# Kernel tuning notes

Hardware: AMD Instinct MI355X
Metric: run time of the kernel (lower is better)

The kernel has to match this reference:

```python
import jax, jax.numpy as jnp
import numpy as np

A, S, D, V = 128, 512, 768, 30522
NL, LW = 10, 5  # n label categories, words per category
MASK_ID = 103
NEG = -1e30


def setup_inputs() -> dict:
    key = jax.random.key(0)
    ks = jax.random.split(key, 12)
    scale = 0.02
    input_ids = jax.random.randint(ks[0], (A, S), 0, 30000)
    input_ids = jnp.where(input_ids == MASK_ID, MASK_ID + 1, input_ids)  # strip accidental masks
    mask_pos = jax.random.randint(ks[1], (A,), 1, 3)  # one [MASK] per row, before position 3
    input_ids = input_ids.at[jnp.arange(A), mask_pos].set(MASK_ID)
    length = jax.random.randint(ks[2], (A,), 1, 400)
    bert_out = jax.random.normal(ks[3], (A, S, D), jnp.float32)
    label_words = jax.random.randint(ks[4], (NL, LW), 0, V)
    return {
        "bert_out": bert_out,
        "input_ids": input_ids,
        "length": length,
        "label_words": label_words,
        "W_senti": jax.random.normal(ks[5], (2, D), jnp.float32) * scale,
        "b_senti": jnp.zeros((2,), jnp.float32),
        "W_dense": jax.random.normal(ks[6], (D, 2 * D), jnp.float32) * scale,
        "b_dense": jnp.zeros((D,), jnp.float32),
        "W_prob": jax.random.normal(ks[7], (V, D), jnp.float32) * scale,
        "b_prob": jnp.zeros((V,), jnp.float32),
        "W_lab": jax.random.normal(ks[8], (NL, 2, LW), jnp.float32) * scale,
    }


def reference(bert_out, input_ids, length, label_words,
              W_senti, b_senti, W_dense, b_dense, W_prob, b_prob, W_lab):
    a, s, d = bert_out.shape
    # pooler = [CLS] hidden state -> senti head (dropout is identity in eval)
    senti_out = bert_out[:, 0] @ W_senti.T + b_senti  # [A,2]

    # gather the (single) [MASK] token hidden state per sample
    mask_pos = jnp.argmax(input_ids == MASK_ID, axis=1)        # [A]
    mask_logit = bert_out[jnp.arange(a), mask_pos]             # [A,D]

    # ragged attention pool over bert_out[i, 3:3+length[i]] vectorized via masking
    pos = jnp.arange(s)
    valid = (pos[None, :] >= 3) & (pos[None, :] < 3 + length[:, None])  # [A,S]
    scores = jnp.einsum('asd,ad->as', bert_out, mask_logit)
    scores = jnp.where(valid, scores, NEG)
    w = jax.nn.softmax(scores, axis=1)                         # [A,S]
    att = jnp.einsum('as,asd->ad', w, bert_out)                # [A,D]

    x = jnp.concatenate([att, mask_logit], axis=-1)            # [A,2D]
    h = jnp.tanh(x @ W_dense.T + b_dense)                      # [A,D]
    p = jnp.tanh(h @ W_prob.T + b_prob)                        # [A,V]

    # per-category label-word gather + small no-bias linear, stacked on dim 2
    lp = p[:, label_words]                                     # [A,NL,LW]
    out = jnp.einsum('alw,lkw->akl', lp, W_lab)                # [A,2,NL]
    return senti_out, out
```

## Files before the change

### kernel.cpp

```cpp
#include <hip/hip_runtime.h>
#include <stdint.h>

#define A_ 128
#define S_ 512
#define D_ 768
#define MASKID 103

typedef short bf16x8_t __attribute__((ext_vector_type(8)));
typedef float floatx4_t __attribute__((ext_vector_type(4)));

__device__ __forceinline__ unsigned short f2bf(float f) {
    union { unsigned int u; float f; } v; v.f = f;
    unsigned int u = v.u;
    return (unsigned short)((u + 0x7fffu + ((u >> 16) & 1u)) >> 16);
}

__global__ __launch_bounds__(512) void attn_fused(
    const float* __restrict__ bert,
    const int* __restrict__ ids,
    const int* __restrict__ length,
    const int* __restrict__ label_words,
    const float* __restrict__ W_prob,
    const float* __restrict__ b_prob,
    const float* __restrict__ W_senti,
    const float* __restrict__ b_senti,
    unsigned short* __restrict__ ws_Wpw,
    float* __restrict__ ws_bp,
    unsigned short* __restrict__ ws_x,
    float* __restrict__ d_out)
{
    int bx = blockIdx.x;
    int tid = threadIdx.x;
    if (bx >= A_) {
        int r = bx - A_;
        if (r < 50) {
            int word = label_words[r];
            const float* src = W_prob + (size_t)word * D_;
            for (int j = tid; j < D_; j += 512) ws_Wpw[r * D_ + j] = f2bf(src[j]);
            if (tid == 0) ws_bp[r] = b_prob[word];
        } else {
            for (int j = tid; j < D_; j += 512) ws_Wpw[r * D_ + j] = 0;
            if (tid == 0) ws_bp[r] = 0.f;
        }
        return;
    }
    int a = bx;
    int wave = tid >> 6, lane = tid & 63;
    int d0 = lane * 12;

    __shared__ int s_minpos;
    __shared__ float red_m[8], red_l[8];
    __shared__ float red_acc[8][D_];
    __shared__ float s0[8], s1[8];

    if (tid == 0) s_minpos = S_;
    __syncthreads();
    if (ids[a * S_ + tid] == MASKID) atomicMin(&s_minpos, tid);
    __syncthreads();
    int mp = (s_minpos >= S_) ? 0 : s_minpos;

    const float* base = bert + (size_t)a * S_ * D_;

    float ml[12];
    {
        const float4* p = (const float4*)(base + (size_t)mp * D_ + d0);
        float4 v0 = p[0], v1 = p[1], v2 = p[2];
        ml[0]=v0.x; ml[1]=v0.y; ml[2]=v0.z; ml[3]=v0.w;
        ml[4]=v1.x; ml[5]=v1.y; ml[6]=v1.z; ml[7]=v1.w;
        ml[8]=v2.x; ml[9]=v2.y; ml[10]=v2.z; ml[11]=v2.w;
    }
    int len = length[a]; if (len > S_ - 3) len = S_ - 3;

    float m = -3.0e38f, l = 0.f;
    float acc[12];
#pragma unroll
    for (int k = 0; k < 12; k++) acc[k] = 0.f;

    for (int v = wave; v < len; v += 8) {
        int s = 3 + v;
        const float4* p = (const float4*)(base + (size_t)s * D_ + d0);
        float4 v0 = p[0], v1 = p[1], v2 = p[2];
        float r[12];
        r[0]=v0.x; r[1]=v0.y; r[2]=v0.z; r[3]=v0.w;
        r[4]=v1.x; r[5]=v1.y; r[6]=v1.z; r[7]=v1.w;
        r[8]=v2.x; r[9]=v2.y; r[10]=v2.z; r[11]=v2.w;
        float part = 0.f;
#pragma unroll
        for (int k = 0; k < 12; k++) part = fmaf(r[k], ml[k], part);
#pragma unroll
        for (int off = 32; off >= 1; off >>= 1)
            part += __shfl_xor(part, off, 64);
        float mn = fmaxf(m, part);
        float alpha = __expf(m - mn);
        float wgt = __expf(part - mn);
        l = l * alpha + wgt;
#pragma unroll
        for (int k = 0; k < 12; k++) acc[k] = fmaf(acc[k], alpha, wgt * r[k]);
        m = mn;
    }
    if (lane == 0) { red_m[wave] = m; red_l[wave] = l; }
#pragma unroll
    for (int k = 0; k < 12; k++) red_acc[wave][d0 + k] = acc[k];

    float p0 = 0.f, p1 = 0.f;
    for (int d = tid; d < D_; d += 512) {
        float b = base[d];
        p0 = fmaf(b, W_senti[d], p0);
        p1 = fmaf(b, W_senti[D_ + d], p1);
    }
#pragma unroll
    for (int off = 32; off >= 1; off >>= 1) {
        p0 += __shfl_xor(p0, off, 64);
        p1 += __shfl_xor(p1, off, 64);
    }
    if (lane == 0) { s0[wave] = p0; s1[wave] = p1; }
    __syncthreads();

    float M = red_m[0];
#pragma unroll
    for (int c = 1; c < 8; c++) M = fmaxf(M, red_m[c]);
    float fac[8]; float denom = 0.f;
#pragma unroll
    for (int c = 0; c < 8; c++) { fac[c] = __expf(red_m[c] - M); denom += fac[c] * red_l[c]; }
    float inv = 1.0f / fmaxf(denom, 1e-30f);

    const float* mrow = base + (size_t)mp * D_;
    for (int d = tid; d < D_; d += 512) {
        float s = 0.f;
#pragma unroll
        for (int c = 0; c < 8; c++) s += fac[c] * red_acc[c][d];
        ws_x[a * 1536 + d] = f2bf(s * inv);
        ws_x[a * 1536 + D_ + d] = f2bf(mrow[d]);
    }
    if (tid == 0) {
        float t0 = b_senti[0], t1 = b_senti[1];
#pragma unroll
        for (int c = 0; c < 8; c++) { t0 += s0[c]; t1 += s1[c]; }
        d_out[a * 2 + 0] = t0;
        d_out[a * 2 + 1] = t1;
    }
}

__global__ __launch_bounds__(256) void dense_kernel(
    const unsigned short* __restrict__ ws_x,
    const float* __restrict__ W_dense,
    const float* __restrict__ b_dense,
    unsigned short* __restrict__ ws_h)
{
    int tid = threadIdx.x;
    int wave = tid >> 6, lane = tid & 63;
    int r = lane & 15, q = lane >> 4;
    int tile_local = wave >> 1, kh = wave & 1;
    int T = blockIdx.x * 2 + tile_local;
    int m_t = T / 48, n_t = T % 48;
    const bf16x8_t* Ap = (const bf16x8_t*)(ws_x + (size_t)(m_t * 16 + r) * 1536 + kh * 768 + q * 8);
    const float* Bp = W_dense + (size_t)(n_t * 16 + r) * 1536 + kh * 768 + q * 8;
    floatx4_t acc = {0.f, 0.f, 0.f, 0.f};
#pragma unroll
    for (int kk = 0; kk < 24; kk++) {
        bf16x8_t av = Ap[kk * 4];
        float4 b0 = *(const float4*)(Bp + kk * 32);
        float4 b1 = *(const float4*)(Bp + kk * 32 + 4);
        bf16x8_t bv;
        bv[0] = (short)f2bf(b0.x); bv[1] = (short)f2bf(b0.y);
        bv[2] = (short)f2bf(b0.z); bv[3] = (short)f2bf(b0.w);
        bv[4] = (short)f2bf(b1.x); bv[5] = (short)f2bf(b1.y);
        bv[6] = (short)f2bf(b1.z); bv[7] = (short)f2bf(b1.w);
        acc = __builtin_amdgcn_mfma_f32_16x16x32_bf16(av, bv, acc, 0, 0, 0);
    }
    __shared__ float part[4][256];
#pragma unroll
    for (int reg = 0; reg < 4; reg++)
        part[wave][(q * 4 + reg) * 16 + r] = acc[reg];
    __syncthreads();
    for (int t = tid; t < 512; t += 256) {
        int tl = t >> 8, id2 = t & 255;
        float sum = part[tl * 2][id2] + part[tl * 2 + 1][id2];
        int T2 = blockIdx.x * 2 + tl;
        int mt2 = T2 / 48, nt2 = T2 % 48;
        int row = id2 >> 4, col = id2 & 15;
        int n = nt2 * 16 + col;
        float h = tanhf(sum + b_dense[n]);
        ws_h[(size_t)(mt2 * 16 + row) * 768 + n] = f2bf(h);
    }
}

__global__ __launch_bounds__(256) void label_kernel(
    const unsigned short* __restrict__ ws_h,
    const unsigned short* __restrict__ ws_Wpw,
    const float* __restrict__ ws_bp,
    const float* __restrict__ W_lab,
    float* __restrict__ d_out)
{
    int tid = threadIdx.x;
    int wave = tid >> 6, lane = tid & 63;
    int r = lane & 15, q = lane >> 4;
    int m_t = blockIdx.x;
    int n_t = wave;
    const bf16x8_t* Ap = (const bf16x8_t*)(ws_h + (size_t)(m_t * 16 + r) * 768 + q * 8);
    const bf16x8_t* Bp = (const bf16x8_t*)(ws_Wpw + (size_t)(n_t * 16 + r) * 768 + q * 8);
    floatx4_t acc = {0.f, 0.f, 0.f, 0.f};
#pragma unroll
    for (int kk = 0; kk < 24; kk++)
        acc = __builtin_amdgcn_mfma_f32_16x16x32_bf16(Ap[kk * 4], Bp[kk * 4], acc, 0, 0, 0);
    __shared__ float lp_s[16][64];
    int col = n_t * 16 + r;
    float bp = ws_bp[col];
#pragma unroll
    for (int reg = 0; reg < 4; reg++)
        lp_s[q * 4 + reg][col] = tanhf(acc[reg] + bp);
    __syncthreads();
    for (int t = tid; t < 320; t += 256) {
        int al = t / 20, rem = t % 20;
        int k = rem / 10, lb = rem % 10;
        float s = 0.f;
#pragma unroll
        for (int w = 0; w < 5; w++)
            s = fmaf(lp_s[al][lb * 5 + w], W_lab[(lb * 2 + k) * 5 + w], s);
        d_out[256 + (m_t * 16 + al) * 20 + rem] = s;
    }
}

extern "C" void kernel_launch(void* const* d_in, const int* in_sizes, int n_in,
                              void* d_out, int out_size, void* d_ws, size_t ws_size,
                              hipStream_t stream) {
    const float* bert    = (const float*)d_in[0];
    const int* ids       = (const int*)d_in[1];
    const int* length    = (const int*)d_in[2];
    const int* label_words = (const int*)d_in[3];
    const float* W_senti = (const float*)d_in[4];
    const float* b_senti = (const float*)d_in[5];
    const float* W_dense = (const float*)d_in[6];
    const float* b_dense = (const float*)d_in[7];
    const float* W_prob  = (const float*)d_in[8];
    const float* b_prob  = (const float*)d_in[9];
    const float* W_lab   = (const float*)d_in[10];
    float* out = (float*)d_out;

    char* ws = (char*)d_ws;
    unsigned short* ws_x   = (unsigned short*)(ws + 0);
    unsigned short* ws_h   = (unsigned short*)(ws + 393216);
    unsigned short* ws_Wpw = (unsigned short*)(ws + 589824);
    float*          ws_bp  = (float*)(ws + 688128);

    attn_fused<<<A_ + 64, 512, 0, stream>>>(bert, ids, length, label_words,
        W_prob, b_prob, W_senti, b_senti, ws_Wpw, ws_bp, ws_x, out);
    dense_kernel<<<192, 256, 0, stream>>>(ws_x, W_dense, b_dense, ws_h);
    label_kernel<<<8, 256, 0, stream>>>(ws_h, ws_Wpw, ws_bp, W_lab, out);
}
```

Measured before the change: 337.2 us.

## Split attention pooling across eight blocks per sample with a merge kernel

Splits each sample's ragged attention pool across 8 blocks of 256 threads (split-K flash-decoding style) instead of one 512-thread block per sample. Each block writes partial max, sum and accumulator to workspace, and a new merge kernel combines them and also computes the senti head. The aim is to fill the GPU's compute units while streaming bert_out, which 128 blocks cannot do. The cost is an extra kernel launch and a workspace round-trip for the partials, plus redundant mask-position scans in every split block.

```diff
diff --git a/kernel.cpp b/kernel.cpp
--- a/kernel.cpp
+++ b/kernel.cpp
@@ -15,47 +15,47 @@
     return (unsigned short)((u + 0x7fffu + ((u >> 16) & 1u)) >> 16);
 }
 
-__global__ __launch_bounds__(512) void attn_fused(
+__global__ __launch_bounds__(256) void attn_part(
     const float* __restrict__ bert,
     const int* __restrict__ ids,
     const int* __restrict__ length,
     const int* __restrict__ label_words,
     const float* __restrict__ W_prob,
     const float* __restrict__ b_prob,
-    const float* __restrict__ W_senti,
-    const float* __restrict__ b_senti,
     unsigned short* __restrict__ ws_Wpw,
     float* __restrict__ ws_bp,
-    unsigned short* __restrict__ ws_x,
-    float* __restrict__ d_out)
+    int* __restrict__ ws_mask_pos,
+    float* __restrict__ part_m,
+    float* __restrict__ part_l,
+    float* __restrict__ part_acc)
 {
     int bx = blockIdx.x;
     int tid = threadIdx.x;
-    if (bx >= A_) {
-        int r = bx - A_;
+    if (bx >= A_ * 8) {
+        int r = bx - A_ * 8;
         if (r < 50) {
             int word = label_words[r];
             const float* src = W_prob + (size_t)word * D_;
-            for (int j = tid; j < D_; j += 512) ws_Wpw[r * D_ + j] = f2bf(src[j]);
+            for (int j = tid; j < D_; j += 256) ws_Wpw[r * D_ + j] = f2bf(src[j]);
             if (tid == 0) ws_bp[r] = b_prob[word];
         } else {
-            for (int j = tid; j < D_; j += 512) ws_Wpw[r * D_ + j] = 0;
+            for (int j = tid; j < D_; j += 256) ws_Wpw[r * D_ + j] = 0;
             if (tid == 0) ws_bp[r] = 0.f;
         }
         return;
     }
-    int a = bx;
+    int a = bx >> 3, c = bx & 7;
     int wave = tid >> 6, lane = tid & 63;
     int d0 = lane * 12;
 
     __shared__ int s_minpos;
-    __shared__ float red_m[8], red_l[8];
-    __shared__ float red_acc[8][D_];
-    __shared__ float s0[8], s1[8];
+    __shared__ float red_m[4], red_l[4];
+    __shared__ float red_acc[4][D_];
 
     if (tid == 0) s_minpos = S_;
     __syncthreads();
-    if (ids[a * S_ + tid] == MASKID) atomicMin(&s_minpos, tid);
+    for (int p = tid; p < S_; p += 256)
+        if (ids[a * S_ + p] == MASKID) atomicMin(&s_minpos, p);
     __syncthreads();
     int mp = (s_minpos >= S_) ? 0 : s_minpos;
 
@@ -76,7 +76,7 @@
 #pragma unroll
     for (int k = 0; k < 12; k++) acc[k] = 0.f;
 
-    for (int v = wave; v < len; v += 8) {
+    for (int v = c + 8 * wave; v < len; v += 32) {
         int s = 3 + v;
         const float4* p = (const float4*)(base + (size_t)s * D_ + d0);
         float4 v0 = p[0], v1 = p[1], v2 = p[2];
@@ -101,10 +101,67 @@
     if (lane == 0) { red_m[wave] = m; red_l[wave] = l; }
 #pragma unroll
     for (int k = 0; k < 12; k++) red_acc[wave][d0 + k] = acc[k];
-
+    __syncthreads();
+
+    float m0 = red_m[0], m1 = red_m[1], m2 = red_m[2], m3 = red_m[3];
+    float M = fmaxf(fmaxf(m0, m1), fmaxf(m2, m3));
+    float f0 = __expf(m0 - M), f1 = __expf(m1 - M);
+    float f2 = __expf(m2 - M), f3 = __expf(m3 - M);
+    int pc = (a * 8 + c) * D_;
+#pragma unroll
+    for (int e = 0; e < 3; e++) {
+        int d = tid + 256 * e;
+        part_acc[pc + d] = f0 * red_acc[0][d] + f1 * red_acc[1][d]
+                         + f2 * red_acc[2][d] + f3 * red_acc[3][d];
+    }
+    if (tid == 0) {
+        part_m[a * 8 + c] = M;
+        part_l[a * 8 + c] = f0 * red_l[0] + f1 * red_l[1] + f2 * red_l[2] + f3 * red_l[3];
+        if (c == 0) ws_mask_pos[a] = mp;
+    }
+}
+
+__global__ __launch_bounds__(256) void merge_kernel(
+    const float* __restrict__ bert,
+    const float* __restrict__ W_senti,
+    const float* __restrict__ b_senti,
+    const int* __restrict__ ws_mask_pos,
+    const float* __restrict__ part_m,
+    const float* __restrict__ part_l,
+    const float* __restrict__ part_acc,
+    unsigned short* __restrict__ ws_x,
+    float* __restrict__ d_out)
+{
+    int a = blockIdx.x, tid = threadIdx.x;
+    float mc[8], lc[8];
+#pragma unroll
+    for (int c = 0; c < 8; c++) { mc[c] = part_m[a * 8 + c]; lc[c] = part_l[a * 8 + c]; }
+    float M = mc[0];
+#pragma unroll
+    for (int c = 1; c < 8; c++) M = fmaxf(M, mc[c]);
+    float fac[8]; float denom = 0.f;
+#pragma unroll
+    for (int c = 0; c < 8; c++) { fac[c] = __expf(mc[c] - M); denom += fac[c] * lc[c]; }
+    float inv = 1.0f / fmaxf(denom, 1e-30f);
+
+    const float* pa = part_acc + (size_t)a * 8 * D_;
+    int mp = ws_mask_pos[a];
+    const float* mrow = bert + ((size_t)a * S_ + mp) * D_;
+#pragma unroll
+    for (int e = 0; e < 3; e++) {
+        int d = tid + 256 * e;
+        float s = 0.f;
+#pragma unroll
+        for (int c = 0; c < 8; c++) s += fac[c] * pa[c * D_ + d];
+        ws_x[a * 1536 + d] = f2bf(s * inv);
+        ws_x[a * 1536 + D_ + d] = f2bf(mrow[d]);
+    }
+    const float* r0 = bert + (size_t)a * S_ * D_;
     float p0 = 0.f, p1 = 0.f;
-    for (int d = tid; d < D_; d += 512) {
-        float b = base[d];
+#pragma unroll
+    for (int e = 0; e < 3; e++) {
+        int d = tid + 256 * e;
+        float b = r0[d];
         p0 = fmaf(b, W_senti[d], p0);
         p1 = fmaf(b, W_senti[D_ + d], p1);
     }
@@ -113,31 +170,13 @@
         p0 += __shfl_xor(p0, off, 64);
         p1 += __shfl_xor(p1, off, 64);
     }
+    __shared__ float s0[4], s1[4];
+    int wave = tid >> 6, lane = tid & 63;
     if (lane == 0) { s0[wave] = p0; s1[wave] = p1; }
     __syncthreads();
-
-    float M = red_m[0];
-#pragma unroll
-    for (int c = 1; c < 8; c++) M = fmaxf(M, red_m[c]);
-    float fac[8]; float denom = 0.f;
-#pragma unroll
-    for (int c = 0; c < 8; c++) { fac[c] = __expf(red_m[c] - M); denom += fac[c] * red_l[c]; }
-    float inv = 1.0f / fmaxf(denom, 1e-30f);
-
-    const float* mrow = base + (size_t)mp * D_;
-    for (int d = tid; d < D_; d += 512) {
-        float s = 0.f;
-#pragma unroll
-        for (int c = 0; c < 8; c++) s += fac[c] * red_acc[c][d];
-        ws_x[a * 1536 + d] = f2bf(s * inv);
-        ws_x[a * 1536 + D_ + d] = f2bf(mrow[d]);
-    }
     if (tid == 0) {
-        float t0 = b_senti[0], t1 = b_senti[1];
-#pragma unroll
-        for (int c = 0; c < 8; c++) { t0 += s0[c]; t1 += s1[c]; }
-        d_out[a * 2 + 0] = t0;
-        d_out[a * 2 + 1] = t1;
+        d_out[a * 2 + 0] = s0[0] + s0[1] + s0[2] + s0[3] + b_senti[0];
+        d_out[a * 2 + 1] = s1[0] + s1[1] + s1[2] + s1[3] + b_senti[1];
     }
 }
 
@@ -242,9 +281,15 @@
     unsigned short* ws_h   = (unsigned short*)(ws + 393216);
     unsigned short* ws_Wpw = (unsigned short*)(ws + 589824);
     float*          ws_bp  = (float*)(ws + 688128);
-
-    attn_fused<<<A_ + 64, 512, 0, stream>>>(bert, ids, length, label_words,
-        W_prob, b_prob, W_senti, b_senti, ws_Wpw, ws_bp, ws_x, out);
+    int*     ws_mask_pos   = (int*)(ws + 688384);
+    float*          part_m = (float*)(ws + 688896);
+    float*          part_l = (float*)(ws + 692992);
+    float*        part_acc = (float*)(ws + 697088);
+
+    attn_part<<<A_ * 8 + 64, 256, 0, stream>>>(bert, ids, length, label_words,
+        W_prob, b_prob, ws_Wpw, ws_bp, ws_mask_pos, part_m, part_l, part_acc);
+    merge_kernel<<<A_, 256, 0, stream>>>(bert, W_senti, b_senti, ws_mask_pos,
+        part_m, part_l, part_acc, ws_x, out);
     dense_kernel<<<192, 256, 0, stream>>>(ws_x, W_dense, b_dense, ws_h);
     label_kernel<<<8, 256, 0, stream>>>(ws_h, ws_Wpw, ws_bp, W_lab, out);
 }
```

Result: faster. 326.7 us (-3.1%).
